# Kernel tuning notes

Hardware: AMD Instinct MI355X
Metric: run time of the kernel (lower is better)

Reference implementation:

```python
import jax, jax.numpy as jnp
import numpy as np

N, E, De, Dv = 40000, 8000, 32, 8   # nodes, hyperedges, edge degree, node degree
D, Q, EIG, VOC, NC = 256, 256, 64, 1000, 40  # vertex/edge dim, query dim, eig dim, centrality vocab, classes
LN_EPS = 1e-5


def _linear(x, W, b):
    return x @ W + b


def _layernorm(x, g, b):
    mu = jnp.mean(x, axis=-1, keepdims=True)
    var = jnp.mean(jnp.square(x - mu), axis=-1, keepdims=True)
    return (x - mu) * jax.lax.rsqrt(var + LN_EPS) * g + b


def setup_inputs() -> dict:
    key = jax.random.key(0)
    ks = iter(jax.random.split(key, 64))
    def nrm(shape, s=0.02):
        return (jax.random.normal(next(ks), shape, jnp.float32) * s).astype(jnp.float32)
    inp = {
        'vfeat': jax.random.normal(next(ks), (N, D), jnp.float32),
        'efeat': jax.random.normal(next(ks), (E, D), jnp.float32),
        'eign_vec': jax.random.normal(next(ks), (N, EIG), jnp.float32),
        'feat_v_gcn': jax.random.normal(next(ks), (N, D), jnp.float32),
        'cent1': jax.random.uniform(next(ks), (E, De), jnp.float32),
        'cent2': jax.random.uniform(next(ks), (N, Dv), jnp.float32),
        'cent_idx': jax.random.randint(next(ks), (N,), 0, VOC),
        'uniq_idx': jax.random.randint(next(ks), (N,), 0, VOC),
        'edge2node': jax.random.randint(next(ks), (E, De), 0, N),
        'node2edge': jax.random.randint(next(ks), (N, Dv), 0, E),
        # learned parameters (W: [in, out])
        'W_vtx': nrm((D, D)), 'b_vtx': jnp.zeros((D,), jnp.float32),
        'W_pe': nrm((EIG, D)), 'b_pe': jnp.zeros((D,), jnp.float32),
        'cs_emb': nrm((VOC, D)), 'un_emb': nrm((VOC, D)),
        'W_kv': nrm((D, Q)), 'b_kv': jnp.zeros((Q,), jnp.float32),
        'W_vv': nrm((D, D)), 'b_vv': jnp.zeros((D,), jnp.float32),
        'W_qe': nrm((D, Q)), 'b_qe': jnp.zeros((Q,), jnp.float32),
        'W_ke': nrm((D, Q)), 'b_ke': jnp.zeros((Q,), jnp.float32),
        'W_ve': nrm((D, D)), 'b_ve': jnp.zeros((D,), jnp.float32),
        'W_qv': nrm((D, Q)), 'b_qv': jnp.zeros((Q,), jnp.float32),
        'W_l1': nrm((D, Q)), 'b_l1': jnp.zeros((Q,), jnp.float32),
        'W_l2': nrm((Q, D)), 'b_l2': jnp.zeros((D,), jnp.float32),
        'W_l3': nrm((D, Q)), 'b_l3': jnp.zeros((Q,), jnp.float32),
        'W_l4': nrm((Q, D)), 'b_l4': jnp.zeros((D,), jnp.float32),
        'ln1_g': jnp.ones((D,), jnp.float32), 'ln1_b': jnp.zeros((D,), jnp.float32),
        'ln2_g': jnp.ones((D,), jnp.float32), 'ln2_b': jnp.zeros((D,), jnp.float32),
        'W_cls': nrm((D, NC)), 'b_cls': jnp.zeros((NC,), jnp.float32),
    }
    return inp


def _forward(vfeat, efeat, eign_vec, feat_v_gcn, cent1, cent2,
             W_vtx, b_vtx, W_pe, b_pe, cs_emb, un_emb,
             W_kv, b_kv, W_vv, b_vv, W_qe, b_qe, W_ke, b_ke, W_ve, b_ve, W_qv, b_qv,
             W_l1, b_l1, W_l2, b_l2, W_l3, b_l3, W_l4, b_l4,
             ln1_g, ln1_b, ln2_g, ln2_b, W_cls, b_cls,
             cent_idx, uniq_idx, edge2node, node2edge):
    scale = 1.0 / np.sqrt(float(W_kv.shape[1]))  # 1/sqrt(query_dim)
    # first_layer feature assembly: vtx_lin_1layer + PE + GCN + centrality/uniqueness embeddings
    feat_v = (_linear(vfeat, W_vtx, b_vtx) + _linear(eign_vec, W_pe, b_pe)
              + feat_v_gcn + cs_emb[cent_idx] + un_emb[uniq_idx])
    feat_e = efeat

    # ---- stage 1: hyperedges attend over member nodes ('in' etype) ----
    k_n = _linear(feat_v, W_kv, b_kv)              # [N,Q]
    v_n = _linear(feat_v, W_vv, b_vv)              # [N,D]
    q_e = _linear(feat_e, W_qe, b_qe)              # [E,Q]
    km = k_n[edge2node]                            # [E,De,Q]
    attn = jax.nn.leaky_relu(jnp.einsum('edq,eq->ed', km, q_e), 0.01) * scale
    score = jax.nn.softmax(attn + cent1, axis=1)   # centrality-biased softmax (k-core + clustering)
    h_e = jnp.einsum('ed,edc->ec', score, v_n[edge2node])  # [E,D]
    x_e = _layernorm(h_e + feat_e, ln1_g, ln1_b)
    f_e = _linear(jax.nn.relu(_linear(x_e, W_l1, b_l1)), W_l2, b_l2)
    feat_e = _layernorm(f_e + x_e, ln1_g, ln1_b)

    # ---- stage 2: nodes attend over incident hyperedges ('con' etype) ----
    k_e = _linear(feat_e, W_ke, b_ke)              # [E,Q]
    v_e = _linear(feat_e, W_ve, b_ve)              # [E,D]
    q_v = _linear(feat_v, W_qv, b_qv)              # [N,Q]
    km2 = k_e[node2edge]                           # [N,Dv,Q]
    attn2 = jax.nn.leaky_relu(jnp.einsum('ndq,nq->nd', km2, q_v), 0.01) * scale
    score2 = jax.nn.softmax(attn2 + cent2, axis=1)
    h_v = jnp.einsum('nd,ndc->nc', score2, v_e[node2edge])  # [N,D]
    x_v = _layernorm(h_v + feat_v, ln2_g, ln2_b)
    f_v = _linear(jax.nn.relu(_linear(x_v, W_l3, b_l3)), W_l4, b_l4)
    feat_v = _layernorm(f_v + x_v, ln2_g, ln2_b)

    # last_layer classification head (dropout is identity in eval)
    return _linear(feat_v, W_cls, b_cls)           # [N,NC]


def reference(vfeat, efeat, eign_vec, feat_v_gcn, cent1, cent2,
              cent_idx, uniq_idx, edge2node, node2edge,
              W_vtx, b_vtx, W_pe, b_pe, cs_emb, un_emb,
              W_kv, b_kv, W_vv, b_vv, W_qe, b_qe, W_ke, b_ke, W_ve, b_ve, W_qv, b_qv,
              W_l1, b_l1, W_l2, b_l2, W_l3, b_l3, W_l4, b_l4,
              ln1_g, ln1_b, ln2_g, ln2_b, W_cls, b_cls):
    return _forward(vfeat, efeat, eign_vec, feat_v_gcn, cent1, cent2,
                    W_vtx, b_vtx, W_pe, b_pe, cs_emb, un_emb,
                    W_kv, b_kv, W_vv, b_vv, W_qe, b_qe, W_ke, b_ke, W_ve, b_ve, W_qv, b_qv,
                    W_l1, b_l1, W_l2, b_l2, W_l3, b_l3, W_l4, b_l4,
                    ln1_g, ln1_b, ln2_g, ln2_b, W_cls, b_cls,
                    cent_idx, uniq_idx, edge2node, node2edge)
```

## Files before the change

kernel.cpp:

```cpp
#include <hip/hip_runtime.h>
#include <hip/hip_bf16.h>
#include <cstddef>

#define N_NODES 40000
#define N_EDGES 8000
#define DE 32
#define DV 8
#define DIM 256
#define QDIM 256
#define EIGD 64
#define NCLS 40
#define LN_EPS 1e-5f
#define ATT_SCALE 0.0625f

typedef unsigned short u16;
typedef unsigned int u32;
typedef unsigned char u8;
using i16x8 = __attribute__((ext_vector_type(8))) short;
using f32x4 = __attribute__((ext_vector_type(4))) float;
using f32x2 = __attribute__((ext_vector_type(2))) float;

__device__ inline u16 f2b(float f) {
    union { float f; u32 u; } c; c.f = f;
    u32 u = c.u + 0x7FFF + ((c.u >> 16) & 1);
    return (u16)(u >> 16);
}
__device__ inline float b2f(u16 b) {
    union { u32 u; float f; } c; c.u = (u32)b << 16;
    return c.f;
}

__device__ inline void f8x4_to_f32(u32 w, float o[4]) {
#if __has_builtin(__builtin_amdgcn_cvt_pk_f32_fp8)
    f32x2 lo = __builtin_amdgcn_cvt_pk_f32_fp8((int)w, false);
    f32x2 hi = __builtin_amdgcn_cvt_pk_f32_fp8((int)w, true);
    o[0] = lo[0]; o[1] = lo[1]; o[2] = hi[0]; o[3] = hi[1];
#else
    f32x2 lo, hi;
    u32 wh = w >> 16;
    asm("v_cvt_pk_f32_fp8 %0, %1" : "=v"(lo) : "v"(w));
    asm("v_cvt_pk_f32_fp8 %0, %1" : "=v"(hi) : "v"(wh));
    o[0] = lo[0]; o[1] = lo[1]; o[2] = hi[0]; o[3] = hi[1];
#endif
}

__device__ inline u32 f8pk2(float a, float b) {
#if __has_builtin(__builtin_amdgcn_cvt_pk_fp8_f32)
    return (u32)__builtin_amdgcn_cvt_pk_fp8_f32(a, b, 0, false) & 0xffffu;
#else
    u32 d = 0;
    asm("v_cvt_pk_fp8_f32 %0, %1, %2" : "+v"(d) : "v"(a), "v"(b));
    return d & 0xffffu;
#endif
}

__device__ inline void gload_lds16(const u16* g, u16* l) {
    __builtin_amdgcn_global_load_lds(
        (const __attribute__((address_space(1))) void*)g,
        (__attribute__((address_space(3))) void*)l, 16, 0, 0);
}

#define VMCNT12 asm volatile("s_waitcnt vmcnt(12)" ::: "memory")
#define VMCNT6  asm volatile("s_waitcnt vmcnt(6)" ::: "memory")
#define VMCNT0  asm volatile("s_waitcnt vmcnt(0)" ::: "memory")
#define LGKM0   asm volatile("s_waitcnt lgkmcnt(0)" ::: "memory")
#define SCHED0  __builtin_amdgcn_sched_barrier(0)
#define SBAR    __builtin_amdgcn_s_barrier()

__global__ __launch_bounds__(256) void prep_weights(
    const float* w0, const float* w1, const float* w2, const float* w3,
    const float* w4, const float* w5, const float* w6, const float* w7,
    const float* w8, const float* w9, const float* w10, const float* w11,
    const float* w12, u16* __restrict__ pool)
{
    const float* srcs[13] = {w0,w1,w2,w3,w4,w5,w6,w7,w8,w9,w10,w11,w12};
    const int Ks[13]  = {256,64,256,256,256,256,256,256,256,256,256,256,256};
    const int Nds[13] = {256,256,256,256,256,256,256,256,256,256,256,256,40};
    const int id = blockIdx.z;
    const float* W = srcs[id];
    u16* Wt = pool + (size_t)id * 65536;
    const int K = Ks[id], Nd = Nds[id];
    const int k0 = blockIdx.x * 32, n0 = blockIdx.y * 32;
    if (k0 >= K || n0 >= Nd) return;

    __shared__ float tile[32][33];
    const int x = threadIdx.x & 31, y4 = (threadIdx.x >> 5) * 4;
#pragma unroll
    for (int j = 0; j < 4; j++) {
        int k = k0 + y4 + j;
        tile[y4 + j][x] = (k < K && (n0 + x) < Nd) ? W[(size_t)k * Nd + n0 + x] : 0.f;
    }
    __syncthreads();
#pragma unroll
    for (int j = 0; j < 4; j++) {
        int n = n0 + y4 + j;
        if (n < Nd && (k0 + x) < K)
            Wt[(size_t)n * K + k0 + x] = f2b(tile[x][y4 + j]);
    }
}

#define MST 264
__global__ __launch_bounds__(256, 2) void asm_kvq(
    const float* __restrict__ vfeat, const float* __restrict__ eign,
    const u16* __restrict__ Wt_vtx, const u16* __restrict__ Wt_pe,
    const float* __restrict__ b_vtx, const float* __restrict__ b_pe,
    const float* __restrict__ gcn, const float* __restrict__ emb1,
    const float* __restrict__ emb2, const int* __restrict__ idx1,
    const int* __restrict__ idx2,
    const u16* __restrict__ Wt_kvq, const float* __restrict__ b_kv,
    const float* __restrict__ b_vv, const float* __restrict__ b_qv,
    u16* __restrict__ FVb, u8* __restrict__ KV8n, u16* __restrict__ QVb)
{
    __shared__ __align__(16) u16 Asm[2][64 * 32];
    __shared__ __align__(16) u16 Bsm[2][256 * 32];
    __shared__ __align__(16) u16 Msm[64 * MST];
    const int t = threadIdx.x;
    const int lane = t & 63, w = t >> 6;
    const int row0 = blockIdx.x * 64;

    const int srow = lane >> 2;
    const int sblk = ((lane & 3) ^ ((lane >> 3) & 3)) * 8;
    const int fr = lane & 15, h = lane >> 4;
    const int rsw = (fr >> 1) & 3;

    f32x4 acc[4][4] = {};
    float4 fA[2][2];

    auto p1_issueB = [&](int kt) {
        const int buf = kt & 1;
        const int k0 = kt << 5;
        const bool tail = (k0 >= 256);
#pragma unroll
        for (int i = 0; i < 4; i++) {
            const int r = w * 64 + i * 16;
            const u16* gp = tail ? Wt_pe + (size_t)(r + srow) * 64 + (k0 - 256) + sblk
                                 : Wt_vtx + (size_t)(r + srow) * 256 + k0 + sblk;
            gload_lds16(gp, &Bsm[buf][r * 32]);
        }
    };
    auto p1_loadA = [&](int kt) {
        const int k0 = kt << 5;
        const bool tail = (k0 >= 256);
        const float* ap = tail
            ? eign + (size_t)(row0 + w * 16 + srow) * 64 + (k0 - 256) + sblk
            : vfeat + (size_t)(row0 + w * 16 + srow) * 256 + k0 + sblk;
        fA[kt & 1][0] = *(const float4*)ap;
        fA[kt & 1][1] = *(const float4*)(ap + 4);
    };
    auto p1_write = [&](int kt) {
        const int buf = kt & 1;
        float4 f0 = fA[buf][0], f1 = fA[buf][1];
        i16x8 v;
        v[0] = (short)f2b(f0.x); v[1] = (short)f2b(f0.y);
        v[2] = (short)f2b(f0.z); v[3] = (short)f2b(f0.w);
        v[4] = (short)f2b(f1.x); v[5] = (short)f2b(f1.y);
        v[6] = (short)f2b(f1.z); v[7] = (short)f2b(f1.w);
        *(i16x8*)&Asm[buf][(w * 16 + srow) * 32 + (lane & 3) * 8] = v;
    };

    p1_loadA(0); p1_issueB(0); p1_loadA(1); p1_write(0);
#pragma unroll
    for (int kt = 0; kt < 10; ++kt) {
        const int buf = kt & 1;
        if (kt + 1 < 10) p1_issueB(kt + 1);
        if (kt + 2 < 10) p1_loadA(kt + 2);
        if (kt + 1 < 10) p1_write(kt + 1);
        else { VMCNT0; }
        LGKM0;
        SBAR;

        i16x8 af[4], bfr[4];
#pragma unroll
        for (int m = 0; m < 4; m++)
            af[m] = *(const i16x8*)&Asm[buf][(m * 16 + fr) * 32 + (h ^ rsw) * 8];
#pragma unroll
        for (int n = 0; n < 4; n++)
            bfr[n] = *(const i16x8*)&Bsm[buf][(w * 64 + n * 16 + fr) * 32 + (h ^ rsw) * 8];
        LGKM0;
        SCHED0;
        SBAR;

#pragma unroll
        for (int m = 0; m < 4; m++)
#pragma unroll
            for (int n = 0; n < 4; n++)
                acc[m][n] = __builtin_amdgcn_mfma_f32_16x16x32_bf16(
                    af[m], bfr[n], acc[m][n], 0, 0, 0);
    }

#pragma unroll
    for (int m = 0; m < 4; m++)
#pragma unroll
        for (int j = 0; j < 4; j++) {
            const int row = m * 16 + h * 4 + j;
#pragma unroll
            for (int n = 0; n < 4; n++) {
                const int col = w * 64 + n * 16 + fr;
                float v = acc[m][n][j] + b_vtx[col] + b_pe[col];
                Msm[row * MST + col] = f2b(v);
            }
        }
    __syncthreads();

    const float4* gcn4 = (const float4*)gcn;
    const float4* e1_4 = (const float4*)emb1;
    const float4* e2_4 = (const float4*)emb2;
    ushort4* FVb4 = (ushort4*)FVb;
#pragma unroll 4
    for (int it = 0; it < 16; ++it) {
        const int T = t + it * 256;
        const int row = T >> 6, cg = T & 63;
        const int grow = row0 + row;
        const int i1 = idx1[grow], i2 = idx2[grow];
        ushort4 mv = *(const ushort4*)&Msm[row * MST + cg * 4];
        float4 gv = gcn4[(size_t)grow * 64 + cg];
        float4 e1 = e1_4[(size_t)i1 * 64 + cg];
        float4 e2 = e2_4[(size_t)i2 * 64 + cg];
        ushort4 o;
        o.x = f2b(b2f(mv.x) + gv.x + e1.x + e2.x);
        o.y = f2b(b2f(mv.y) + gv.y + e1.y + e2.y);
        o.z = f2b(b2f(mv.z) + gv.z + e1.z + e2.z);
        o.w = f2b(b2f(mv.w) + gv.w + e1.w + e2.w);
        FVb4[(size_t)grow * 64 + cg] = o;
        *(ushort4*)&Msm[row * MST + cg * 4] = o;
    }
    __syncthreads();

    auto p2_issueB = [&](int buf, int kt, const u16* Wb) {
#pragma unroll
        for (int i = 0; i < 4; i++) {
            const int r = w * 64 + i * 16;
            gload_lds16(Wb + (size_t)(r + srow) * 256 + (kt << 5) + sblk,
                        &Bsm[buf][r * 32]);
        }
    };
    p2_issueB(0, 0, Wt_kvq);
    VMCNT0; SBAR;
#pragma unroll 1
    for (int c = 0; c < 3; ++c) {
        const u16* Wb = Wt_kvq + (size_t)c * 65536;
        const float* bc = (c == 0) ? b_kv : ((c == 1) ? b_vv : b_qv);
#pragma unroll
        for (int m = 0; m < 4; m++)
#pragma unroll
            for (int n = 0; n < 4; n++)
                acc[m][n] = f32x4{0.f, 0.f, 0.f, 0.f};
#pragma unroll
        for (int kt = 0; kt < 8; ++kt) {
            const int buf = kt & 1;
            if (kt < 7) p2_issueB(buf ^ 1, kt + 1, Wb);
            else if (c < 2) p2_issueB(0, 0, Wb + 65536);

            i16x8 af[4], bfr[4];
#pragma unroll
            for (int m = 0; m < 4; m++)
                af[m] = *(const i16x8*)&Msm[(m * 16 + fr) * MST + (kt << 5) + h * 8];
#pragma unroll
            for (int n = 0; n < 4; n++)
                bfr[n] = *(const i16x8*)&Bsm[buf][(w * 64 + n * 16 + fr) * 32 + (h ^ rsw) * 8];
            LGKM0;
            SCHED0;
#pragma unroll
            for (int m = 0; m < 4; m++)
#pragma unroll
                for (int n = 0; n < 4; n++)
                    acc[m][n] = __builtin_amdgcn_mfma_f32_16x16x32_bf16(
                        af[m], bfr[n], acc[m][n], 0, 0, 0);
            if (kt < 7) { VMCNT0; SBAR; }
        }
        if (c < 2) {
#pragma unroll
            for (int m = 0; m < 4; m++) {
                const size_t rbase = (size_t)(row0 + m * 16 + h * 4) * 512 + c * 256;
#pragma unroll
                for (int n = 0; n < 4; n++) {
                    const int gcol = w * 64 + n * 16 + fr;
                    const float bcv = bc[gcol];
                    u32 p01 = f8pk2(acc[m][n][0] + bcv, acc[m][n][1] + bcv);
                    u32 p23 = f8pk2(acc[m][n][2] + bcv, acc[m][n][3] + bcv);
                    KV8n[rbase + gcol]        = (u8)p01;
                    KV8n[rbase + 512 + gcol]  = (u8)(p01 >> 8);
                    KV8n[rbase + 1024 + gcol] = (u8)p23;
                    KV8n[rbase + 1536 + gcol] = (u8)(p23 >> 8);
                }
            }
        } else {
#pragma unroll
            for (int m = 0; m < 4; m++)
#pragma unroll
                for (int j = 0; j < 4; j++) {
                    const int grow = row0 + m * 16 + h * 4 + j;
#pragma unroll
                    for (int n = 0; n < 4; n++) {
                        const int gcol = w * 64 + n * 16 + fr;
                        QVb[(size_t)grow * 256 + gcol] = f2b(acc[m][n][j] + bc[gcol]);
                    }
                }
        }
        if (c < 2) { VMCNT0; SBAR; }
    }
}

template <int EPI, int AMODE, int NT>
__global__ __launch_bounds__(256, 2) void gemmN(
    const void* __restrict__ Av, const u16* __restrict__ Wt,
    const float* __restrict__ bias0, const float* __restrict__ bias1,
    const float* __restrict__ bias2,
    void* __restrict__ Cv, int Nd)
{
    __shared__ u16 Asm[3][64 * 64];
    __shared__ u16 Bsm[3][128 * 64];
    const int t = threadIdx.x;
    const int lane = t & 63, w = t >> 6;
    const int wr = w >> 1, wc = w & 1;
    const int row0 = blockIdx.y * 64, col0 = blockIdx.x * 128;

    f32x4 acc[2][4] = {};

    const int srow = lane >> 3;
    const int sblk = ((lane & 7) ^ srow) * 8;
    const int fr = lane & 15, h = lane >> 4;
    const int lsw = fr & 7;

    float4 farA[2][2][2];

    auto stage_load = [&](int kt) {
        const int buf = kt % 3;
        const int k0 = kt << 6;
        if constexpr (AMODE == 0) {
#pragma unroll
            for (int i = 0; i < 2; i++) {
                const int r = w * 16 + i * 8;
                gload_lds16((const u16*)Av + (size_t)(row0 + r + srow) * 256 + k0 + sblk,
                            &Asm[buf][r * 64]);
            }
        } else {
#pragma unroll
            for (int i = 0; i < 2; i++) {
                const int r = w * 16 + i * 8;
                const float* ap = (const float*)Av + (size_t)(row0 + r + srow) * 256 + k0 + sblk;
                farA[kt & 1][i][0] = *(const float4*)ap;
                farA[kt & 1][i][1] = *(const float4*)(ap + 4);
            }
        }
#pragma unroll
        for (int i = 0; i < 4; i++) {
            const int r = w * 32 + i * 8;
            int ng = col0 + r + srow; if (ng > Nd - 1) ng = Nd - 1;
            gload_lds16(Wt + (size_t)ng * 256 + k0 + sblk, &Bsm[buf][r * 64]);
        }
    };
    auto stage_write = [&](int kt) {
        const int buf = kt % 3;
#pragma unroll
        for (int i = 0; i < 2; i++) {
            const int r = w * 16 + i * 8;
            float4 f0 = farA[kt & 1][i][0], f1 = farA[kt & 1][i][1];
            i16x8 v;
            v[0] = (short)f2b(f0.x); v[1] = (short)f2b(f0.y);
            v[2] = (short)f2b(f0.z); v[3] = (short)f2b(f0.w);
            v[4] = (short)f2b(f1.x); v[5] = (short)f2b(f1.y);
            v[6] = (short)f2b(f1.z); v[7] = (short)f2b(f1.w);
            *(i16x8*)&Asm[buf][(r + srow) * 64 + (lane & 7) * 8] = v;
        }
    };

    stage_load(0);
    if (NT > 1) stage_load(1);
    if constexpr (AMODE != 0) stage_write(0);

#pragma unroll
    for (int kt = 0; kt < NT; ++kt) {
        const int buf = kt % 3;
        if (kt + 2 < NT) stage_load(kt + 2);
        if constexpr (AMODE != 0) {
            if (kt + 1 < NT) stage_write(kt + 1);
            else { VMCNT0; }
        } else {
            if (kt + 2 < NT) { VMCNT12; }
            else if (kt + 1 < NT) { VMCNT6; }
            else { VMCNT0; }
        }
        LGKM0;
        SBAR;

        i16x8 af[2][2], bfr[2][4];
#pragma unroll
        for (int kk = 0; kk < 2; kk++) {
#pragma unroll
            for (int m = 0; m < 2; m++)
                af[kk][m] = *(const i16x8*)&Asm[buf][(wr * 32 + m * 16 + fr) * 64 +
                                                    ((kk * 4 + h) ^ lsw) * 8];
#pragma unroll
            for (int n = 0; n < 4; n++)
                bfr[kk][n] = *(const i16x8*)&Bsm[buf][(wc * 64 + n * 16 + fr) * 64 +
                                                     ((kk * 4 + h) ^ lsw) * 8];
        }
        LGKM0;
        SCHED0;
        SBAR;

#pragma unroll
        for (int kk = 0; kk < 2; kk++)
#pragma unroll
            for (int m = 0; m < 2; m++)
#pragma unroll
                for (int n = 0; n < 4; n++)
                    acc[m][n] = __builtin_amdgcn_mfma_f32_16x16x32_bf16(
                        af[kk][m], bfr[kk][n], acc[m][n], 0, 0, 0);
    }

    const int seg = (int)(blockIdx.x >> 1);
    const float* bp = (seg == 0) ? bias0 : ((seg == 1) ? bias1 : bias2);
#pragma unroll
    for (int m = 0; m < 2; m++) {
#pragma unroll
        for (int j = 0; j < 4; j++) {
            const int grow = row0 + wr * 32 + m * 16 + h * 4 + j;
#pragma unroll
            for (int n = 0; n < 4; n++) {
                const int gcol = col0 + wc * 64 + n * 16 + fr;
                if (EPI == 4 && gcol >= Nd) continue;
                float v = acc[m][n][j] + bp[gcol & 255];
                if constexpr (EPI == 1) v = fmaxf(v, 0.f);
                if constexpr (EPI == 4)
                    ((float*)Cv)[(size_t)grow * Nd + gcol] = v;
                else
                    ((u16*)Cv)[(size_t)grow * Nd + gcol] = f2b(v);
            }
        }
    }
}

template <int TAIL>
__global__ __launch_bounds__(256, 2) void ffn_fused(
    const u16* __restrict__ X, const u16* __restrict__ Wt1,
    const float* __restrict__ b1, const u16* __restrict__ Wt2,
    const float* __restrict__ b2, const float* __restrict__ lng,
    const float* __restrict__ lnb, const u16* __restrict__ WtT,
    const float* __restrict__ bT0, const float* __restrict__ bT1,
    void* __restrict__ outp)
{
    __shared__ __align__(16) u16 Asm[2][64 * 32];
    __shared__ __align__(16) u16 Bsm[2][256 * 32];
    __shared__ __align__(16) u16 Msm[64 * MST];
    const int t = threadIdx.x;
    const int lane = t & 63, w = t >> 6;
    const int row0 = blockIdx.x * 64;

    const int srow = lane >> 2;
    const int sblk = ((lane & 3) ^ ((lane >> 3) & 3)) * 8;
    const int fr = lane & 15, h = lane >> 4;
    const int rsw = (fr >> 1) & 3;

    f32x4 acc[4][4] = {};

    auto stageA = [&](int buf, int kt) {
        gload_lds16(X + (size_t)(row0 + w * 16 + srow) * 256 + (kt << 5) + sblk,
                    &Asm[buf][(w * 16) * 32]);
    };
    auto stageB = [&](int buf, int kt, const u16* W) {
#pragma unroll
        for (int i = 0; i < 4; i++) {
            const int r = w * 64 + i * 16;
            gload_lds16(W + (size_t)(r + srow) * 256 + (kt << 5) + sblk,
                        &Bsm[buf][r * 32]);
        }
    };

    stageA(0, 0); stageB(0, 0, Wt1);
    VMCNT0; SBAR;
#pragma unroll
    for (int kt = 0; kt < 8; ++kt) {
        const int buf = kt & 1;
        if (kt < 7) { stageA(buf ^ 1, kt + 1); stageB(buf ^ 1, kt + 1, Wt1); }
        else        { stageB(0, 0, Wt2); }

        i16x8 af[4], bfr[4];
#pragma unroll
        for (int m = 0; m < 4; m++)
            af[m] = *(const i16x8*)&Asm[buf][(m * 16 + fr) * 32 + (h ^ rsw) * 8];
#pragma unroll
        for (int n = 0; n < 4; n++)
            bfr[n] = *(const i16x8*)&Bsm[buf][(w * 64 + n * 16 + fr) * 32 + (h ^ rsw) * 8];
        LGKM0;
        SCHED0;
#pragma unroll
        for (int m = 0; m < 4; m++)
#pragma unroll
            for (int n = 0; n < 4; n++)
                acc[m][n] = __builtin_amdgcn_mfma_f32_16x16x32_bf16(
                    af[m], bfr[n], acc[m][n], 0, 0, 0);
        if (kt < 7) { VMCNT0; SBAR; }
    }
    {
        float b1v[4];
#pragma unroll
        for (int n = 0; n < 4; n++) b1v[n] = b1[w * 64 + n * 16 + fr];
#pragma unroll
        for (int m = 0; m < 4; m++)
#pragma unroll
            for (int j = 0; j < 4; j++) {
                const int row = m * 16 + h * 4 + j;
#pragma unroll
                for (int n = 0; n < 4; n++) {
                    const int col = w * 64 + n * 16 + fr;
                    float v = fmaxf(acc[m][n][j] + b1v[n], 0.f);
                    Msm[row * MST + col] = f2b(v);
                    acc[m][n][j] = 0.f;
                }
            }
    }
    __syncthreads();

#pragma unroll
    for (int kt = 0; kt < 8; ++kt) {
        const int buf = kt & 1;
        if (kt < 7) stageB(buf ^ 1, kt + 1, Wt2);
        else if (TAIL == 0) stageB(0, 0, WtT);

        i16x8 af[4], bfr[4];
#pragma unroll
        for (int m = 0; m < 4; m++)
            af[m] = *(const i16x8*)&Msm[(m * 16 + fr) * MST + (kt << 5) + h * 8];
#pragma unroll
        for (int n = 0; n < 4; n++)
            bfr[n] = *(const i16x8*)&Bsm[buf][(w * 64 + n * 16 + fr) * 32 + (h ^ rsw) * 8];
        LGKM0;
        SCHED0;
#pragma unroll
        for (int m = 0; m < 4; m++)
#pragma unroll
            for (int n = 0; n < 4; n++)
                acc[m][n] = __builtin_amdgcn_mfma_f32_16x16x32_bf16(
                    af[m], bfr[n], acc[m][n], 0, 0, 0);
        if (kt < 7) { VMCNT0; SBAR; }
    }
    {
        float* redS = (float*)&Asm[0][0];
        float* redQ = redS + 256;
#pragma unroll
        for (int m = 0; m < 4; m++) {
#pragma unroll
            for (int j = 0; j < 4; j++) {
                const int grow = row0 + m * 16 + h * 4 + j;
                float s = 0.f, q = 0.f;
#pragma unroll
                for (int n = 0; n < 4; n++) {
                    const int gcol = w * 64 + n * 16 + fr;
                    float v = acc[m][n][j] + b2[gcol] +
                              b2f(X[(size_t)grow * 256 + gcol]);
                    acc[m][n][j] = v;
                    s += v; q += v * v;
                }
#pragma unroll
                for (int off = 1; off < 16; off <<= 1) {
                    s += __shfl_xor(s, off, 64);
                    q += __shfl_xor(q, off, 64);
                }
                if (fr == 0) {
                    redS[(m * 16 + h * 4 + j) * 4 + w] = s;
                    redQ[(m * 16 + h * 4 + j) * 4 + w] = q;
                }
            }
        }
        __syncthreads();
#pragma unroll
        for (int m = 0; m < 4; m++) {
#pragma unroll
            for (int j = 0; j < 4; j++) {
                const int r = m * 16 + h * 4 + j;
                float4 s4 = *(const float4*)&redS[r * 4];
                float4 q4 = *(const float4*)&redQ[r * 4];
                float mu = (s4.x + s4.y + s4.z + s4.w) * (1.f / DIM);
                float var = (q4.x + q4.y + q4.z + q4.w) * (1.f / DIM) - mu * mu;
                float rr = rsqrtf(var + LN_EPS);
#pragma unroll
                for (int n = 0; n < 4; n++) {
                    const int gcol = w * 64 + n * 16 + fr;
                    float y = (acc[m][n][j] - mu) * rr * lng[gcol] + lnb[gcol];
                    acc[m][n][j] = y;
                }
            }
        }
        __syncthreads();
#pragma unroll
        for (int m = 0; m < 4; m++)
#pragma unroll
            for (int j = 0; j < 4; j++) {
                const int row = m * 16 + h * 4 + j;
#pragma unroll
                for (int n = 0; n < 4; n++)
                    Msm[row * MST + (w * 64 + n * 16 + fr)] = f2b(acc[m][n][j]);
            }
    }
    __syncthreads();

    if constexpr (TAIL == 0) {
        u8* KV8e = (u8*)outp;
#pragma unroll 1
        for (int half = 0; half < 2; half++) {
            const u16* Wb = WtT + (size_t)half * 65536;
            const float* bT = half ? bT1 : bT0;
#pragma unroll
            for (int m = 0; m < 4; m++)
#pragma unroll
                for (int n = 0; n < 4; n++)
                    acc[m][n] = f32x4{0.f, 0.f, 0.f, 0.f};
#pragma unroll
            for (int kt = 0; kt < 8; ++kt) {
                const int buf = kt & 1;
                if (kt < 7) stageB(buf ^ 1, kt + 1, Wb);
                else if (half == 0) stageB(0, 0, WtT + 65536);

                i16x8 af[4], bfr[4];
#pragma unroll
                for (int m = 0; m < 4; m++)
                    af[m] = *(const i16x8*)&Msm[(m * 16 + fr) * MST + (kt << 5) + h * 8];
#pragma unroll
                for (int n = 0; n < 4; n++)
                    bfr[n] = *(const i16x8*)&Bsm[buf][(w * 64 + n * 16 + fr) * 32 + (h ^ rsw) * 8];
                LGKM0;
                SCHED0;
#pragma unroll
                for (int m = 0; m < 4; m++)
#pragma unroll
                    for (int n = 0; n < 4; n++)
                        acc[m][n] = __builtin_amdgcn_mfma_f32_16x16x32_bf16(
                            af[m], bfr[n], acc[m][n], 0, 0, 0);
                if (kt < 7) { VMCNT0; SBAR; }
            }
#pragma unroll
            for (int m = 0; m < 4; m++) {
                const size_t rbase = (size_t)(row0 + m * 16 + h * 4) * 512 + half * 256;
#pragma unroll
                for (int n = 0; n < 4; n++) {
                    const int gcol = w * 64 + n * 16 + fr;
                    const float bTv = bT[gcol];
                    u32 p01 = f8pk2(acc[m][n][0] + bTv, acc[m][n][1] + bTv);
                    u32 p23 = f8pk2(acc[m][n][2] + bTv, acc[m][n][3] + bTv);
                    KV8e[rbase + gcol]        = (u8)p01;
                    KV8e[rbase + 512 + gcol]  = (u8)(p01 >> 8);
                    KV8e[rbase + 1024 + gcol] = (u8)p23;
                    KV8e[rbase + 1536 + gcol] = (u8)(p23 >> 8);
                }
            }
            if (half == 0) { VMCNT0; SBAR; }
        }
    } else {
        float* out = (float*)outp;
        f32x4 acc3[3] = {};
#pragma unroll
        for (int kk = 0; kk < 8; kk++) {
            i16x8 af = *(const i16x8*)&Msm[(w * 16 + fr) * MST + kk * 32 + h * 8];
#pragma unroll
            for (int n = 0; n < 3; n++) {
                int br = n * 16 + fr; if (br > NCLS - 1) br = NCLS - 1;
                i16x8 bfr = *(const i16x8*)(WtT + (size_t)br * 256 + kk * 32 + h * 8);
                acc3[n] = __builtin_amdgcn_mfma_f32_16x16x32_bf16(af, bfr, acc3[n], 0, 0, 0);
            }
        }
#pragma unroll
        for (int n = 0; n < 3; n++) {
            const int gcol = n * 16 + fr;
            if (gcol >= NCLS) continue;
#pragma unroll
            for (int j = 0; j < 4; j++) {
                const int grow = row0 + w * 16 + h * 4 + j;
                out[(size_t)grow * NCLS + gcol] = acc3[n][j] + bT0[gcol];
            }
        }
    }
}

__global__ __launch_bounds__(256) void edge_attn(
    const u8* __restrict__ KV8n, const u16* __restrict__ QE,
    const float* __restrict__ efeat,
    const int* __restrict__ e2n, const float* __restrict__ cent1,
    const float* __restrict__ g, const float* __restrict__ bb,
    u16* __restrict__ XE)
{
    const int lane = threadIdx.x & 63, w = threadIdx.x >> 6;
    const int e = blockIdx.x * 4 + w;
    const int c4 = lane * 4;

    ushort4 q4 = *(const ushort4*)&QE[(size_t)e * QDIM + c4];
    const float q0 = b2f(q4.x), q1 = b2f(q4.y), q2 = b2f(q4.z), q3 = b2f(q4.w);

    int4 rv[8];
#pragma unroll
    for (int i = 0; i < 8; i++)
        rv[i] = *(const int4*)&e2n[(size_t)e * DE + i * 4];
    int rows[DE];
#pragma unroll
    for (int i = 0; i < 8; i++) {
        rows[i * 4 + 0] = rv[i].x; rows[i * 4 + 1] = rv[i].y;
        rows[i * 4 + 2] = rv[i].z; rows[i * 4 + 3] = rv[i].w;
    }

    float p[DE];
#pragma unroll
    for (int g0 = 0; g0 < DE; g0 += 16) {
        u32 kw[16];
#pragma unroll
        for (int j = 0; j < 16; j++)
            kw[j] = *(const u32*)(KV8n + (size_t)rows[g0 + j] * 512 + c4);
#pragma unroll
        for (int j = 0; j < 16; j++) {
            float kf[4]; f8x4_to_f32(kw[j], kf);
            p[g0 + j] = q0 * kf[0] + q1 * kf[1] + q2 * kf[2] + q3 * kf[3];
        }
    }
#pragma unroll
    for (int off = 32; off; off >>= 1)
#pragma unroll
        for (int d = 0; d < DE; d++)
            p[d] += __shfl_xor(p[d], off, 64);

    float4 cv[8];
#pragma unroll
    for (int i = 0; i < 8; i++)
        cv[i] = *(const float4*)&cent1[(size_t)e * DE + i * 4];
    float cent[DE];
#pragma unroll
    for (int i = 0; i < 8; i++) {
        cent[i * 4 + 0] = cv[i].x; cent[i * 4 + 1] = cv[i].y;
        cent[i * 4 + 2] = cv[i].z; cent[i * 4 + 3] = cv[i].w;
    }
#pragma unroll
    for (int d = 0; d < DE; d++)
        p[d] = (p[d] > 0.f ? p[d] : 0.01f * p[d]) * ATT_SCALE + cent[d];

    float mx = p[0];
#pragma unroll
    for (int d = 1; d < DE; d++) mx = fmaxf(mx, p[d]);
    float s = 0.f;
#pragma unroll
    for (int d = 0; d < DE; d++) { p[d] = __expf(p[d] - mx); s += p[d]; }
    const float inv = 1.f / s;
#pragma unroll
    for (int d = 0; d < DE; d++) p[d] *= inv;

    float a0 = 0.f, a1 = 0.f, a2 = 0.f, a3 = 0.f;
#pragma unroll
    for (int g0 = 0; g0 < DE; g0 += 16) {
        u32 vw[16];
#pragma unroll
        for (int j = 0; j < 16; j++)
            vw[j] = *(const u32*)(KV8n + (size_t)rows[g0 + j] * 512 + 256 + c4);
#pragma unroll
        for (int j = 0; j < 16; j++) {
            float vf[4]; f8x4_to_f32(vw[j], vf);
            const float sd = p[g0 + j];
            a0 = fmaf(sd, vf[0], a0); a1 = fmaf(sd, vf[1], a1);
            a2 = fmaf(sd, vf[2], a2); a3 = fmaf(sd, vf[3], a3);
        }
    }
    float4 ef = *(const float4*)&efeat[(size_t)e * DIM + c4];
    float x0 = a0 + ef.x, x1 = a1 + ef.y, x2 = a2 + ef.z, x3 = a3 + ef.w;

    float mu = x0 + x1 + x2 + x3;
#pragma unroll
    for (int off = 32; off; off >>= 1) mu += __shfl_xor(mu, off, 64);
    mu *= (1.f / DIM);
    float d0 = x0 - mu, d1 = x1 - mu, d2 = x2 - mu, d3 = x3 - mu;
    float var = d0 * d0 + d1 * d1 + d2 * d2 + d3 * d3;
#pragma unroll
    for (int off = 32; off; off >>= 1) var += __shfl_xor(var, off, 64);
    var *= (1.f / DIM);
    float r = rsqrtf(var + LN_EPS);
    float4 gv = *(const float4*)&g[c4];
    float4 bv = *(const float4*)&bb[c4];
    ushort4 o;
    o.x = f2b(d0 * r * gv.x + bv.x); o.y = f2b(d1 * r * gv.y + bv.y);
    o.z = f2b(d2 * r * gv.z + bv.z); o.w = f2b(d3 * r * gv.w + bv.w);
    *(ushort4*)&XE[(size_t)e * DIM + c4] = o;
}

__global__ __launch_bounds__(256) void node_attn(
    const u8* __restrict__ KV8e, const u16* __restrict__ QVb,
    const u16* __restrict__ FV,
    const int* __restrict__ n2e, const float* __restrict__ cent2,
    const float* __restrict__ g, const float* __restrict__ bb,
    u16* __restrict__ XV)
{
    const int lane = threadIdx.x & 63, w = threadIdx.x >> 6;
    const int na = blockIdx.x * 8 + w * 2, nb = na + 1;
    const int c4 = lane * 4;

    ushort4 qa4 = *(const ushort4*)&QVb[(size_t)na * 256 + c4];
    ushort4 qb4 = *(const ushort4*)&QVb[(size_t)nb * 256 + c4];
    const float qa0 = b2f(qa4.x), qa1 = b2f(qa4.y), qa2 = b2f(qa4.z), qa3 = b2f(qa4.w);
    const float qb0 = b2f(qb4.x), qb1 = b2f(qb4.y), qb2 = b2f(qb4.z), qb3 = b2f(qb4.w);

    int4 r0 = *(const int4*)&n2e[(size_t)na * DV];
    int4 r1 = *(const int4*)&n2e[(size_t)na * DV + 4];
    int4 r2 = *(const int4*)&n2e[(size_t)nb * DV];
    int4 r3 = *(const int4*)&n2e[(size_t)nb * DV + 4];
    int rA[8] = {r0.x, r0.y, r0.z, r0.w, r1.x, r1.y, r1.z, r1.w};
    int rB[8] = {r2.x, r2.y, r2.z, r2.w, r3.x, r3.y, r3.z, r3.w};

    u32 kA[8], vA[8], kB[8], vB[8];
#pragma unroll
    for (int d = 0; d < DV; d++) {
        const u8* b = KV8e + (size_t)rA[d] * 512 + c4;
        kA[d] = *(const u32*)b; vA[d] = *(const u32*)(b + 256);
    }
#pragma unroll
    for (int d = 0; d < DV; d++) {
        const u8* b = KV8e + (size_t)rB[d] * 512 + c4;
        kB[d] = *(const u32*)b; vB[d] = *(const u32*)(b + 256);
    }

    float pA[8], pB[8];
#pragma unroll
    for (int d = 0; d < DV; d++) {
        float ka[4], kb[4];
        f8x4_to_f32(kA[d], ka); f8x4_to_f32(kB[d], kb);
        pA[d] = qa0 * ka[0] + qa1 * ka[1] + qa2 * ka[2] + qa3 * ka[3];
        pB[d] = qb0 * kb[0] + qb1 * kb[1] + qb2 * kb[2] + qb3 * kb[3];
    }
#pragma unroll
    for (int off = 32; off; off >>= 1) {
#pragma unroll
        for (int d = 0; d < DV; d++) {
            pA[d] += __shfl_xor(pA[d], off, 64);
            pB[d] += __shfl_xor(pB[d], off, 64);
        }
    }
    float4 cA0 = *(const float4*)&cent2[(size_t)na * DV];
    float4 cA1 = *(const float4*)&cent2[(size_t)na * DV + 4];
    float4 cB0 = *(const float4*)&cent2[(size_t)nb * DV];
    float4 cB1 = *(const float4*)&cent2[(size_t)nb * DV + 4];
    float cA[8] = {cA0.x, cA0.y, cA0.z, cA0.w, cA1.x, cA1.y, cA1.z, cA1.w};
    float cB[8] = {cB0.x, cB0.y, cB0.z, cB0.w, cB1.x, cB1.y, cB1.z, cB1.w};
#pragma unroll
    for (int d = 0; d < DV; d++) {
        pA[d] = (pA[d] > 0.f ? pA[d] : 0.01f * pA[d]) * ATT_SCALE + cA[d];
        pB[d] = (pB[d] > 0.f ? pB[d] : 0.01f * pB[d]) * ATT_SCALE + cB[d];
    }
    float mA = pA[0], mB = pB[0];
#pragma unroll
    for (int d = 1; d < DV; d++) { mA = fmaxf(mA, pA[d]); mB = fmaxf(mB, pB[d]); }
    float sA = 0.f, sB = 0.f;
#pragma unroll
    for (int d = 0; d < DV; d++) {
        pA[d] = __expf(pA[d] - mA); sA += pA[d];
        pB[d] = __expf(pB[d] - mB); sB += pB[d];
    }
    const float iA = 1.f / sA, iB = 1.f / sB;

    float a0 = 0.f, a1 = 0.f, a2 = 0.f, a3 = 0.f;
    float b0 = 0.f, b1 = 0.f, b2 = 0.f, b3 = 0.f;
#pragma unroll
    for (int d = 0; d < DV; d++) {
        float va[4], vb[4];
        f8x4_to_f32(vA[d], va); f8x4_to_f32(vB[d], vb);
        const float sa = pA[d] * iA, sb = pB[d] * iB;
        a0 = fmaf(sa, va[0], a0); a1 = fmaf(sa, va[1], a1);
        a2 = fmaf(sa, va[2], a2); a3 = fmaf(sa, va[3], a3);
        b0 = fmaf(sb, vb[0], b0); b1 = fmaf(sb, vb[1], b1);
        b2 = fmaf(sb, vb[2], b2); b3 = fmaf(sb, vb[3], b3);
    }
    ushort4 fa = *(const ushort4*)&FV[(size_t)na * DIM + c4];
    ushort4 fb = *(const ushort4*)&FV[(size_t)nb * DIM + c4];
    float xa0 = a0 + b2f(fa.x), xa1 = a1 + b2f(fa.y);
    float xa2 = a2 + b2f(fa.z), xa3 = a3 + b2f(fa.w);
    float xb0 = b0 + b2f(fb.x), xb1 = b1 + b2f(fb.y);
    float xb2 = b2 + b2f(fb.z), xb3 = b3 + b2f(fb.w);

    float muA = xa0 + xa1 + xa2 + xa3, muB = xb0 + xb1 + xb2 + xb3;
#pragma unroll
    for (int off = 32; off; off >>= 1) {
        muA += __shfl_xor(muA, off, 64);
        muB += __shfl_xor(muB, off, 64);
    }
    muA *= (1.f / DIM); muB *= (1.f / DIM);
    float da0 = xa0 - muA, da1 = xa1 - muA, da2 = xa2 - muA, da3 = xa3 - muA;
    float db0 = xb0 - muB, db1 = xb1 - muB, db2 = xb2 - muB, db3 = xb3 - muB;
    float vA_ = da0 * da0 + da1 * da1 + da2 * da2 + da3 * da3;
    float vB_ = db0 * db0 + db1 * db1 + db2 * db2 + db3 * db3;
#pragma unroll
    for (int off = 32; off; off >>= 1) {
        vA_ += __shfl_xor(vA_, off, 64);
        vB_ += __shfl_xor(vB_, off, 64);
    }
    const float rA_ = rsqrtf(vA_ * (1.f / DIM) + LN_EPS);
    const float rB_ = rsqrtf(vB_ * (1.f / DIM) + LN_EPS);
    float4 gv = *(const float4*)&g[c4];
    float4 bv = *(const float4*)&bb[c4];
    ushort4 oa, ob;
    oa.x = f2b(da0 * rA_ * gv.x + bv.x); oa.y = f2b(da1 * rA_ * gv.y + bv.y);
    oa.z = f2b(da2 * rA_ * gv.z + bv.z); oa.w = f2b(da3 * rA_ * gv.w + bv.w);
    ob.x = f2b(db0 * rB_ * gv.x + bv.x); ob.y = f2b(db1 * rB_ * gv.y + bv.y);
    ob.z = f2b(db2 * rB_ * gv.z + bv.z); ob.w = f2b(db3 * rB_ * gv.w + bv.w);
    *(ushort4*)&XV[(size_t)na * DIM + c4] = oa;
    *(ushort4*)&XV[(size_t)nb * DIM + c4] = ob;
}

extern "C" void kernel_launch(void* const* d_in, const int* in_sizes, int n_in,
                              void* d_out, int out_size, void* d_ws, size_t ws_size,
                              hipStream_t stream)
{
    const float* vfeat  = (const float*)d_in[0];
    const float* efeat  = (const float*)d_in[1];
    const float* eign   = (const float*)d_in[2];
    const float* gcn    = (const float*)d_in[3];
    const float* cent1  = (const float*)d_in[4];
    const float* cent2  = (const float*)d_in[5];
    const int*   cidx   = (const int*)d_in[6];
    const int*   uidx   = (const int*)d_in[7];
    const int*   e2n    = (const int*)d_in[8];
    const int*   n2e    = (const int*)d_in[9];
    const float* W_vtx  = (const float*)d_in[10]; const float* b_vtx = (const float*)d_in[11];
    const float* W_pe   = (const float*)d_in[12]; const float* b_pe  = (const float*)d_in[13];
    const float* cs_emb = (const float*)d_in[14]; const float* un_emb= (const float*)d_in[15];
    const float* W_kv   = (const float*)d_in[16]; const float* b_kv  = (const float*)d_in[17];
    const float* W_vv   = (const float*)d_in[18]; const float* b_vv  = (const float*)d_in[19];
    const float* W_qe   = (const float*)d_in[20]; const float* b_qe  = (const float*)d_in[21];
    const float* W_ke   = (const float*)d_in[22]; const float* b_ke  = (const float*)d_in[23];
    const float* W_ve   = (const float*)d_in[24]; const float* b_ve  = (const float*)d_in[25];
    const float* W_qv   = (const float*)d_in[26]; const float* b_qv  = (const float*)d_in[27];
    const float* W_l1   = (const float*)d_in[28]; const float* b_l1  = (const float*)d_in[29];
    const float* W_l2   = (const float*)d_in[30]; const float* b_l2  = (const float*)d_in[31];
    const float* W_l3   = (const float*)d_in[32]; const float* b_l3  = (const float*)d_in[33];
    const float* W_l4   = (const float*)d_in[34]; const float* b_l4  = (const float*)d_in[35];
    const float* ln1_g  = (const float*)d_in[36]; const float* ln1_b = (const float*)d_in[37];
    const float* ln2_g  = (const float*)d_in[38]; const float* ln2_b = (const float*)d_in[39];
    const float* W_cls  = (const float*)d_in[40]; const float* b_cls = (const float*)d_in[41];
    float* out = (float*)d_out;

    const size_t NE = (size_t)N_NODES * DIM;
    const size_t EE = (size_t)N_EDGES * DIM;
    u16* ws = (u16*)d_ws;
    u16* FVb  = ws;
    u16* QVb  = FVb + NE;
    u16* B2   = QVb + NE;
    u16* QEb  = B2 + NE;
    u16* XE   = QEb + EE;
    u8*  KV8n = (u8*)(XE + EE);
    u8*  KV8e = KV8n + (size_t)N_NODES * 512;
    u16* Wp   = (u16*)(KV8e + (size_t)N_EDGES * 512);
    u16* Wt_vtx = Wp +  0 * 65536;
    u16* Wt_pe  = Wp +  1 * 65536;
    u16* Wt_kvq = Wp +  2 * 65536;
    u16* Wt_qe  = Wp +  5 * 65536;
    u16* Wt_kve = Wp +  6 * 65536;
    u16* Wt_l1  = Wp +  8 * 65536;
    u16* Wt_l2  = Wp +  9 * 65536;
    u16* Wt_l3  = Wp + 10 * 65536;
    u16* Wt_l4  = Wp + 11 * 65536;
    u16* Wt_cls = Wp + 12 * 65536;

    const dim3 blk(256);
    const dim3 gW(8, 8, 13);
    const dim3 gQE(2, N_EDGES / 64);

    prep_weights<<<gW, blk, 0, stream>>>(
        W_vtx, W_pe, W_kv, W_vv, W_qv, W_qe, W_ke, W_ve,
        W_l1, W_l2, W_l3, W_l4, W_cls, Wp);

    asm_kvq<<<N_NODES / 64, blk, 0, stream>>>(
        vfeat, eign, Wt_vtx, Wt_pe, b_vtx, b_pe,
        gcn, cs_emb, un_emb, cidx, uidx,
        Wt_kvq, b_kv, b_vv, b_qv, FVb, KV8n, QVb);

    gemmN<0, 1, 4><<<gQE, blk, 0, stream>>>(efeat, Wt_qe,
        b_qe, b_qe, b_qe, QEb, 256);
    edge_attn<<<N_EDGES / 4, blk, 0, stream>>>(KV8n, QEb, efeat, e2n, cent1,
        ln1_g, ln1_b, XE);
    ffn_fused<0><<<N_EDGES / 64, blk, 0, stream>>>(XE, Wt_l1, b_l1,
        Wt_l2, b_l2, ln1_g, ln1_b, Wt_kve, b_ke, b_ve, KV8e);

    node_attn<<<N_NODES / 8, blk, 0, stream>>>(KV8e, QVb, FVb, n2e, cent2,
        ln2_g, ln2_b, B2);
    ffn_fused<1><<<N_NODES / 64, blk, 0, stream>>>(B2, Wt_l3, b_l3,
        Wt_l4, b_l4, ln2_g, ln2_b, Wt_cls, b_cls, nullptr, out);
}
```

Measured before the change: 219.3 us.

## Split asm_kvq work across eight waves with narrower per-wave column tiles

Doubles the asm_kvq block from 256 to 512 threads. Each wave now covers 32 output columns instead of 64 and each thread loads one float4 of A per K-step. The aim is more resident waves per CU to hide memory and LDS latency, at the same LDS footprint per block, and fewer accumulator registers per thread. The Msm row stride padding also changes from 264 to 266, which makes LDS rows no longer 16-byte aligned for the vector reads and may cost extra LDS cycles.

```diff
diff --git a/kernel.cpp b/kernel.cpp
--- a/kernel.cpp
+++ b/kernel.cpp
@@ -17,6 +17,7 @@
 typedef unsigned int u32;
 typedef unsigned char u8;
 using i16x8 = __attribute__((ext_vector_type(8))) short;
+using i16x4 = __attribute__((ext_vector_type(4))) short;
 using f32x4 = __attribute__((ext_vector_type(4))) float;
 using f32x2 = __attribute__((ext_vector_type(2))) float;
 
@@ -99,8 +100,8 @@
     }
 }
 
-#define MST 264
-__global__ __launch_bounds__(256, 2) void asm_kvq(
+#define MST 266
+__global__ __launch_bounds__(512, 2) void asm_kvq(
     const float* __restrict__ vfeat, const float* __restrict__ eign,
     const u16* __restrict__ Wt_vtx, const u16* __restrict__ Wt_pe,
     const float* __restrict__ b_vtx, const float* __restrict__ b_pe,
@@ -123,16 +124,21 @@
     const int fr = lane & 15, h = lane >> 4;
     const int rsw = (fr >> 1) & 3;
 
-    f32x4 acc[4][4] = {};
-    float4 fA[2][2];
+    const int arow = w * 8 + (lane >> 3);
+    const int ablk = (lane & 7) >> 1;
+    const int ahalf = lane & 1;
+    const int asrc = ((ablk ^ h) * 8) + ahalf * 4;
+
+    f32x4 acc[4][2] = {};
+    float4 fA[2];
 
     auto p1_issueB = [&](int kt) {
         const int buf = kt & 1;
         const int k0 = kt << 5;
         const bool tail = (k0 >= 256);
 #pragma unroll
-        for (int i = 0; i < 4; i++) {
-            const int r = w * 64 + i * 16;
+        for (int i = 0; i < 2; i++) {
+            const int r = w * 32 + i * 16;
             const u16* gp = tail ? Wt_pe + (size_t)(r + srow) * 64 + (k0 - 256) + sblk
                                  : Wt_vtx + (size_t)(r + srow) * 256 + k0 + sblk;
             gload_lds16(gp, &Bsm[buf][r * 32]);
@@ -142,20 +148,17 @@
         const int k0 = kt << 5;
         const bool tail = (k0 >= 256);
         const float* ap = tail
-            ? eign + (size_t)(row0 + w * 16 + srow) * 64 + (k0 - 256) + sblk
-            : vfeat + (size_t)(row0 + w * 16 + srow) * 256 + k0 + sblk;
-        fA[kt & 1][0] = *(const float4*)ap;
-        fA[kt & 1][1] = *(const float4*)(ap + 4);
+            ? eign + (size_t)(row0 + arow) * 64 + (k0 - 256) + asrc
+            : vfeat + (size_t)(row0 + arow) * 256 + k0 + asrc;
+        fA[kt & 1] = *(const float4*)ap;
     };
     auto p1_write = [&](int kt) {
         const int buf = kt & 1;
-        float4 f0 = fA[buf][0], f1 = fA[buf][1];
-        i16x8 v;
+        float4 f0 = fA[kt & 1];
+        i16x4 v;
         v[0] = (short)f2b(f0.x); v[1] = (short)f2b(f0.y);
         v[2] = (short)f2b(f0.z); v[3] = (short)f2b(f0.w);
-        v[4] = (short)f2b(f1.x); v[5] = (short)f2b(f1.y);
-        v[6] = (short)f2b(f1.z); v[7] = (short)f2b(f1.w);
-        *(i16x8*)&Asm[buf][(w * 16 + srow) * 32 + (lane & 3) * 8] = v;
+        *(i16x4*)&Asm[buf][arow * 32 + ablk * 8 + ahalf * 4] = v;
     };
 
     p1_loadA(0); p1_issueB(0); p1_loadA(1); p1_write(0);
@@ -169,13 +172,13 @@
         LGKM0;
         SBAR;
 
-        i16x8 af[4], bfr[4];
+        i16x8 af[4], bfr[2];
 #pragma unroll
         for (int m = 0; m < 4; m++)
-            af[m] = *(const i16x8*)&Asm[buf][(m * 16 + fr) * 32 + (h ^ rsw) * 8];
-#pragma unroll
-        for (int n = 0; n < 4; n++)
-            bfr[n] = *(const i16x8*)&Bsm[buf][(w * 64 + n * 16 + fr) * 32 + (h ^ rsw) * 8];
+            af[m] = *(const i16x8*)&Asm[buf][(m * 16 + fr) * 32 + ((h ^ rsw)) * 8];
+#pragma unroll
+        for (int n = 0; n < 2; n++)
+            bfr[n] = *(const i16x8*)&Bsm[buf][(w * 32 + n * 16 + fr) * 32 + ((h ^ rsw)) * 8];
         LGKM0;
         SCHED0;
         SBAR;
@@ -183,7 +186,7 @@
 #pragma unroll
         for (int m = 0; m < 4; m++)
 #pragma unroll
-            for (int n = 0; n < 4; n++)
+            for (int n = 0; n < 2; n++)
                 acc[m][n] = __builtin_amdgcn_mfma_f32_16x16x32_bf16(
                     af[m], bfr[n], acc[m][n], 0, 0, 0);
     }
@@ -194,8 +197,8 @@
         for (int j = 0; j < 4; j++) {
             const int row = m * 16 + h * 4 + j;
 #pragma unroll
-            for (int n = 0; n < 4; n++) {
-                const int col = w * 64 + n * 16 + fr;
+            for (int n = 0; n < 2; n++) {
+                const int col = w * 32 + n * 16 + fr;
                 float v = acc[m][n][j] + b_vtx[col] + b_pe[col];
                 Msm[row * MST + col] = f2b(v);
             }
@@ -207,8 +210,8 @@
     const float4* e2_4 = (const float4*)emb2;
     ushort4* FVb4 = (ushort4*)FVb;
 #pragma unroll 4
-    for (int it = 0; it < 16; ++it) {
-        const int T = t + it * 256;
+    for (int it = 0; it < 8; ++it) {
+        const int T = t + it * 512;
         const int row = T >> 6, cg = T & 63;
         const int grow = row0 + row;
         const int i1 = idx1[grow], i2 = idx2[grow];
@@ -228,8 +231,8 @@
 
     auto p2_issueB = [&](int buf, int kt, const u16* Wb) {
 #pragma unroll
-        for (int i = 0; i < 4; i++) {
-            const int r = w * 64 + i * 16;
+        for (int i = 0; i < 2; i++) {
+            const int r = w * 32 + i * 16;
             gload_lds16(Wb + (size_t)(r + srow) * 256 + (kt << 5) + sblk,
                         &Bsm[buf][r * 32]);
         }
@@ -243,7 +246,7 @@
 #pragma unroll
         for (int m = 0; m < 4; m++)
 #pragma unroll
-            for (int n = 0; n < 4; n++)
+            for (int n = 0; n < 2; n++)
                 acc[m][n] = f32x4{0.f, 0.f, 0.f, 0.f};
 #pragma unroll
         for (int kt = 0; kt < 8; ++kt) {
@@ -251,19 +254,19 @@
             if (kt < 7) p2_issueB(buf ^ 1, kt + 1, Wb);
             else if (c < 2) p2_issueB(0, 0, Wb + 65536);
 
-            i16x8 af[4], bfr[4];
+            i16x8 af[4], bfr[2];
 #pragma unroll
             for (int m = 0; m < 4; m++)
                 af[m] = *(const i16x8*)&Msm[(m * 16 + fr) * MST + (kt << 5) + h * 8];
 #pragma unroll
-            for (int n = 0; n < 4; n++)
-                bfr[n] = *(const i16x8*)&Bsm[buf][(w * 64 + n * 16 + fr) * 32 + (h ^ rsw) * 8];
+            for (int n = 0; n < 2; n++)
+                bfr[n] = *(const i16x8*)&Bsm[buf][(w * 32 + n * 16 + fr) * 32 + ((h ^ rsw)) * 8];
             LGKM0;
             SCHED0;
 #pragma unroll
             for (int m = 0; m < 4; m++)
 #pragma unroll
-                for (int n = 0; n < 4; n++)
+                for (int n = 0; n < 2; n++)
                     acc[m][n] = __builtin_amdgcn_mfma_f32_16x16x32_bf16(
                         af[m], bfr[n], acc[m][n], 0, 0, 0);
             if (kt < 7) { VMCNT0; SBAR; }
@@ -273,8 +276,8 @@
             for (int m = 0; m < 4; m++) {
                 const size_t rbase = (size_t)(row0 + m * 16 + h * 4) * 512 + c * 256;
 #pragma unroll
-                for (int n = 0; n < 4; n++) {
-                    const int gcol = w * 64 + n * 16 + fr;
+                for (int n = 0; n < 2; n++) {
+                    const int gcol = w * 32 + n * 16 + fr;
                     const float bcv = bc[gcol];
                     u32 p01 = f8pk2(acc[m][n][0] + bcv, acc[m][n][1] + bcv);
                     u32 p23 = f8pk2(acc[m][n][2] + bcv, acc[m][n][3] + bcv);
@@ -291,8 +294,8 @@
                 for (int j = 0; j < 4; j++) {
                     const int grow = row0 + m * 16 + h * 4 + j;
 #pragma unroll
-                    for (int n = 0; n < 4; n++) {
-                        const int gcol = w * 64 + n * 16 + fr;
+                    for (int n = 0; n < 2; n++) {
+                        const int gcol = w * 32 + n * 16 + fr;
                         QVb[(size_t)grow * 256 + gcol] = f2b(acc[m][n][j] + bc[gcol]);
                     }
                 }
@@ -953,6 +956,7 @@
     u16* Wt_cls = Wp + 12 * 65536;
 
     const dim3 blk(256);
+    const dim3 blk512(512);
     const dim3 gW(8, 8, 13);
     const dim3 gQE(2, N_EDGES / 64);
 
@@ -960,7 +964,7 @@
         W_vtx, W_pe, W_kv, W_vv, W_qv, W_qe, W_ke, W_ve,
         W_l1, W_l2, W_l3, W_l4, W_cls, Wp);
 
-    asm_kvq<<<N_NODES / 64, blk, 0, stream>>>(
+    asm_kvq<<<N_NODES / 64, blk512, 0, stream>>>(
         vfeat, eign, Wt_vtx, Wt_pe, b_vtx, b_pe,
         gcn, cs_emb, un_emb, cidx, uidx,
         Wt_kvq, b_kv, b_vv, b_qv, FVb, KV8n, QVb);
```

After: 222.0 us. No clear change (+1.2%).
